# Performance work log

Measured on AMD Instinct MI355X. Metric: run time of the kernel, lower is better.

The kernel has to match this reference:

```python
import jax, jax.numpy as jnp
import numpy as np

# ---- static hyperparameters (mirror init_kwargs) ----
L_MAX = 3
N_MAX_L = [8, 6, 4, 2]            # radial basis size per l (precomputer.n_max_l)
N_CHANNELS = 32                   # num_element_channels
K_MAX_L = [n * N_CHANNELS for n in N_MAX_L]   # [256, 192, 128, 64]
SH_SIZES = [2 * l + 1 for l in range(L_MAX + 1)]  # [1,3,5,7]
MP_SCALING = 0.1
NU_SCALING = 0.1
NU_MAX = 2                        # max_correlation_order_per_layer
N_LAYERS = 2                      # num_message_passing_layers

# Fixed CG coupling tensors for all valid (l1, l2, L) with |l1-l2|<=L<=min(l1+l2, L_MAX).
# (Deterministic stand-ins for real Clebsch-Gordan coefficients; same sparsity/coupling
# structure and identical in fwd and fwdbwd modules.)
_rng = np.random.RandomState(0)
CG = {}
for _l1 in range(L_MAX + 1):
    for _l2 in range(L_MAX + 1):
        for _L in range(abs(_l1 - _l2), min(_l1 + _l2, L_MAX) + 1):
            CG[(_l1, _l2, _L)] = jnp.asarray(
                (_rng.randn(2 * _l1 + 1, 2 * _l2 + 1, 2 * _L + 1) * 0.2).astype(np.float32))


def split_l(x, sizes):
    out, i = [], 0
    for s in sizes:
        out.append(x[:, i:i + s])
        i += s
    return out


def embed_centers(feats, emb):
    # feats[l]: [N, 2l+1, n_l*C]; multiply channel block c by per-atom embedding emb[:, c]
    C = emb.shape[1]
    out = []
    for f in feats:
        n, m, k = f.shape
        out.append((f.reshape(n, m, k // C, C) * emb[:, None, None, :]).reshape(n, m, k))
    return out


def tensor_product(A, B):
    # per-atom CG tensor product, channel-aligned with truncation to min k
    n = A[0].shape[0]
    out = [jnp.zeros((n, 2 * L + 1, K_MAX_L[L]), A[0].dtype) for L in range(L_MAX + 1)]
    for (l1, l2, L), cg in CG.items():
        kk = min(K_MAX_L[l1], K_MAX_L[l2], K_MAX_L[L])
        t = jnp.einsum('nak,nbk,abM->nMk', A[l1][:, :, :kk], B[l2][:, :, :kk], cg)
        out[L] = out[L].at[:, :, :kk].add(t)
    return out


def cg_iterate(feats):
    # CGIterator: nu_max-1 iterated tensor products with residual accumulation
    g = feats
    for _ in range(NU_MAX - 1):
        tp = tensor_product(g, feats)
        g = [g[l] + NU_SCALING * tp[l] for l in range(L_MAX + 1)]
    return g


def invariant_mp(rb_l, sh_l, centers, emb_nbr, n_atoms):
    # spherical expansion: scatter rb x sh x neighbor-embedding over pairs -> centers
    out = []
    for l in range(L_MAX + 1):
        # [P, 2l+1, n_l, C] -> [P, 2l+1, k_l]
        msg = sh_l[l][:, :, None, None] * rb_l[l][:, None, :, None] * emb_nbr[:, None, None, :]
        msg = msg.reshape(msg.shape[0], 2 * l + 1, -1)
        out.append(MP_SCALING * jax.ops.segment_sum(msg, centers, num_segments=n_atoms))
    return out


def equivariant_mp(rb_l, sh_l, centers, neighbors, feats, n_atoms):
    # pair messages: CG-couple radially weighted SH edge features with neighbor features
    edge = [sh_l[l] * rb_l[l].sum(-1, keepdims=True) for l in range(L_MAX + 1)]  # [P, 2l+1]
    out = [jnp.zeros((n_atoms, 2 * L + 1, K_MAX_L[L]), feats[0].dtype) for L in range(L_MAX + 1)]
    for (l1, l2, L), cg in CG.items():
        kk = min(K_MAX_L[l2], K_MAX_L[L])
        w = jnp.einsum('pa,abM->pbM', edge[l1], cg)        # [P, 2l2+1, 2L+1]
        fg = feats[l2][neighbors, :, :kk]                   # gather: [P, 2l2+1, kk]
        msg = jnp.einsum('pbM,pbk->pMk', w, fg)             # [P, 2L+1, kk]
        out[L] = out[L].at[:, :, :kk].add(
            MP_SCALING * jax.ops.segment_sum(msg, centers, num_segments=n_atoms))
    return out


def setup_inputs() -> dict:
    key = jax.random.key(0)
    ks = jax.random.split(key, 8)
    N, P = 5000, 100000
    return {
        'sh': jax.random.normal(ks[0], (P, sum(SH_SIZES)), dtype=jnp.float32),
        'rb': jax.random.uniform(ks[1], (P, sum(N_MAX_L)), dtype=jnp.float32),
        'emb_table': jax.random.normal(ks[2], (4, N_CHANNELS), dtype=jnp.float32),
        'w_energy': jax.random.normal(ks[3], (K_MAX_L[0], 1), dtype=jnp.float32) * 0.05,
        'b_energy': jax.random.normal(ks[4], (1,), dtype=jnp.float32),
        'species_idx': jax.random.randint(ks[5], (N,), 0, 4, dtype=jnp.int32),
        'centers': jax.random.randint(ks[6], (P,), 0, N, dtype=jnp.int32),
        'neighbors': jax.random.randint(ks[7], (P,), 0, N, dtype=jnp.int32),
    }


def reference(sh, rb, emb_table, w_energy, b_energy, species_idx, centers, neighbors):
    n_atoms = species_idx.shape[0]
    sh_l = split_l(sh * NU_SCALING, SH_SIZES)   # nu_scaling applied to spherical harmonics
    rb_l = split_l(rb, N_MAX_L)
    center_emb = emb_table[species_idx]          # [N, C]
    emb_nbr = center_emb[neighbors]              # [P, C]
    # invariant message passing -> spherical expansion, then first CG iteration
    feats = invariant_mp(rb_l, sh_l, centers, emb_nbr, n_atoms)
    feats = cg_iterate(feats)
    # remaining equivariant message-passing layers
    for _ in range(N_LAYERS - 1):
        ef = embed_centers(feats, center_emb)
        mp = equivariant_mp(rb_l, sh_l, centers, neighbors, ef, n_atoms)
        feats = cg_iterate(mp)
    feats = embed_centers(feats, center_emb)
    energies = feats[0] @ w_energy + b_energy    # [N, 1, 1]
    return energies
```

## Files before the change

kernel.cpp:

```cpp
#include <hip/hip_runtime.h>
#include <vector>
#include <cmath>
#include <cstdint>

constexpr int KLc[4]  = {256,192,128,64};
constexpr int NMLc[4] = {8,6,4,2};
constexpr int SHBc[5] = {0,1,4,9,16};
constexpr int RBBc[5] = {0,8,14,18,20};
constexpr int FBc[5]  = {0,256,832,1472,1920};
constexpr int NCMB = 34, CGTOT = 3436, FTOT = 1920;

struct Combos { int l1[NCMB], l2[NCMB], L[NCMB], cgoff[NCMB], kk[NCMB]; };
constexpr Combos make_combos(){
  Combos c{}; int n=0, cg=0;
  for(int a=0;a<=3;a++)for(int b=0;b<=3;b++){
    int lo=a>b?a-b:b-a, hi=(a+b<3)?(a+b):3;
    for(int L=lo;L<=hi;L++){
      c.l1[n]=a; c.l2[n]=b; c.L[n]=L; c.cgoff[n]=cg;
      int mx=a>b?a:b; if(L>mx) mx=L; c.kk[n]=KLc[mx];
      cg+=(2*a+1)*(2*b+1)*(2*L+1); n++;
    }
  }
  return c;
}
constexpr Combos CB = make_combos();
static_assert(CB.cgoff[NCMB-1] + 7*7*7 == CGTOT, "cg size");

struct Grp { int cnt[4]; int list[4][12]; };
constexpr Grp make_Lg(){ Grp g{}; for(int i=0;i<NCMB;i++){ int L=CB.L[i]; g.list[L][g.cnt[L]++]=i; } return g; }
constexpr Grp LG = make_Lg();

struct Rows { int sh[64], rb[64], off[64]; };
constexpr Rows make_rows(){ Rows r{}; int i=0;
  for(int l=0;l<4;l++)for(int m=0;m<2*l+1;m++)for(int n=0;n<NMLc[l];n++){
    r.sh[i]=SHBc[l]+m; r.rb[i]=RBBc[l]+n; r.off[i]=FBc[l]+m*KLc[l]+n*32; i++; }
  for(;i<64;i++){ r.sh[i]=0; r.rb[i]=0; r.off[i]=0; }
  return r; }
constexpr Rows RWS = make_rows();

constexpr int NSL=425, NG=8, MAXS=56, MAXR=12, RPAD=149;

constexpr int iabs_(int x){ return x<0?-x:x; }
__host__ __device__ constexpr bool sl_valid(int l1,int l2,int kt){ return l2<=3-kt && iabs_(l1-l2)<=3-kt; }

__host__ __device__ constexpr int rb_base(int kt,int l1,int l2){
  int base=0;
  for(int p=0;p<4;p++)for(int q=0;q<4;q++){
    if(p==l1 && q==l2) return base;
    if(sl_valid(p,q,kt)) base += (2*p+1)*(2*q+1);
  }
  return base;
}

struct EqTab {
  int ns[NG];
  unsigned char eidx[NG][MAXS];
  unsigned char fidx[NG][MAXS];
  short         srow[NG][MAXS];
  unsigned char sph [NG][MAXS];
  int nr[NG];
  short roff[NG][MAXR];
  int total;
};
constexpr EqTab make_eqtab(){
  EqTab T{}; int gidx=0;
  for(int l2=0;l2<4;l2++)for(int kt=0;kt<4-l2;kt++)for(int b=0;b<2*l2+1;b++){
    const int rowoff = FBc[l2] + b*KLc[l2] + kt*64;
    for(int l1=0;l1<4;l1++){
      if(!sl_valid(l1,l2,kt)) continue;
      for(int a=0;a<2*l1+1;a++){
        int g = (gidx*NG)/NSL;
        int s = T.ns[g]++;
        T.eidx[g][s] = (unsigned char)(SHBc[l1]+a);
        int rbi = rb_base(kt,l1,l2) + a*(2*l2+1) + b;
        int ph, sr;
        if(kt==0){ if(l1<=2){ ph=0; sr=rbi; } else { ph=1; sr=rbi-144; } }
        else { ph=kt+1; sr=rbi; }
        T.sph[g][s]=(unsigned char)ph; T.srow[g][s]=(short)sr;
        int ri=-1;
        for(int r=0;r<T.nr[g];r++) if(T.roff[g][r]==(short)rowoff) ri=r;
        if(ri<0){ ri=T.nr[g]; T.roff[g][T.nr[g]++]=(short)rowoff; }
        T.fidx[g][s]=(unsigned char)ri;
        gidx++;
      }
    }
  }
  T.total=gidx;
  return T;
}
constexpr EqTab ET = make_eqtab();
static_assert(ET.total==NSL, "slice count");
constexpr bool chk_ns(){ for(int g=0;g<NG;g++) if(ET.ns[g]>MAXS) return false; return true; }
constexpr bool chk_nr(){ for(int g=0;g<NG;g++) if(ET.nr[g]>MAXR) return false; return true; }
static_assert(chk_ns(), "MAXS");
static_assert(chk_nr(), "MAXR");

struct CAsg { int cnt[NG]; unsigned char ci[NG][8]; };
constexpr CAsg make_casg(){
  CAsg C{}; bool used[NCMB]{}; int load[NG]{};
  for(int it=0; it<NCMB; it++){
    int best=-1, bc=-1;
    for(int i=0;i<NCMB;i++) if(!used[i]){
      int c=(2*CB.l1[i]+1)*(2*CB.l2[i]+1)*(2*CB.L[i]+1);
      if(c>bc){bc=c;best=i;}
    }
    used[best]=true;
    int g=0; for(int j=1;j<NG;j++) if(load[j]<load[g]) g=j;
    C.ci[g][C.cnt[g]++]=(unsigned char)best; load[g]+=bc;
  }
  return C;
}
constexpr CAsg CA = make_casg();
constexpr bool chk_ca(){ for(int g=0;g<NG;g++) if(CA.cnt[g]>8) return false; return true; }
static_assert(chk_ca(), "CA cap");

__host__ __device__ constexpr bool combo_in_phase(int ci,int ph){
  int l1=CB.l1[ci], l2=CB.l2[ci], L=CB.L[ci];
  if(ph==0) return l1<=2;
  if(ph==1) return l1==3;
  int kt=ph-1;
  return (l2<=3-kt) && (L<=3-kt);
}
__host__ __device__ constexpr int phase_kt(int ph){ return ph<=1?0:ph-1; }
__host__ __device__ constexpr int phase_rbadj(int ph){ return ph==1?144:0; }

namespace nprng {
struct MT {
  uint32_t mt[624]; int mti; bool has_g; double g;
  void seed(uint32_t s){ for(int i=0;i<624;i++){ mt[i]=s; s=1812433253u*(s^(s>>30))+(uint32_t)i+1u; } mti=624; has_g=false; g=0.0; }
  uint32_t u32(){
    if(mti>=624){
      for(int i=0;i<624;i++){
        uint32_t y=(mt[i]&0x80000000u)|(mt[(i+1)%624]&0x7fffffffu);
        mt[i]=mt[(i+397)%624]^(y>>1)^((y&1u)?0x9908b0dfu:0u);
      }
      mti=0;
    }
    uint32_t y=mt[mti++];
    y^=y>>11; y^=(y<<7)&0x9d2c5680u; y^=(y<<15)&0xefc60000u; y^=y>>18;
    return y;
  }
  double dbl(){ uint32_t a=u32()>>5, b=u32()>>6; return (a*67108864.0+b)/9007199254740992.0; }
  double gauss(){
    if(has_g){ has_g=false; return g; }
    double f,x1,x2,r2;
    do{ x1=2.0*dbl()-1.0; x2=2.0*dbl()-1.0; r2=x1*x1+x2*x2; }while(r2>=1.0||r2==0.0);
    f=sqrt(-2.0*log(r2)/r2);
    g=f*x1; has_g=true; return f*x2;
  }
};
}
static std::vector<float> build_cg(){
  nprng::MT r; r.seed(0);
  std::vector<float> v; v.reserve(CGTOT);
  for(int l1=0;l1<=3;l1++)for(int l2=0;l2<=3;l2++){
    int lo = l1>l2? l1-l2 : l2-l1;
    int hi = (l1+l2<3)? (l1+l2) : 3;
    for(int L=lo;L<=hi;L++){
      int n=(2*l1+1)*(2*l2+1)*(2*L+1);
      for(int i=0;i<n;i++) v.push_back((float)(r.gauss()*0.2));
    }
  }
  return v;
}

__global__ __launch_bounds__(256) void k_cemb(const float* __restrict__ emb_table,
    const int* __restrict__ species, float* __restrict__ cemb, int* __restrict__ counts, int N){
  int i = blockIdx.x*256 + threadIdx.x;
  if(i < N) counts[i] = 0;
  if(i < N*32){ int n = i>>5, c = i&31; cemb[i] = emb_table[species[n]*32 + c]; }
}

__global__ __launch_bounds__(256) void k_hist(const int* __restrict__ centers, int* counts, int P){
  int i = blockIdx.x*256 + threadIdx.x;
  if(i < P) atomicAdd(&counts[centers[i]], 1);
}

__global__ __launch_bounds__(256) void k_scan(const int* __restrict__ counts,
    int* __restrict__ offsets, int* __restrict__ cursor, int N){
  __shared__ int part[256];
  const int t = threadIdx.x;
  const int CH = (N + 255)/256;
  const int lo = t*CH;
  int hi = (t+1)*CH; if(hi > N) hi = N;
  int s = 0;
  for(int i=lo;i<hi;i++) s += counts[i];
  part[t] = s; __syncthreads();
  const int own = s;
  for(int d=1; d<256; d<<=1){
    int v = (t>=d)? part[t-d] : 0;
    __syncthreads();
    part[t] += v;
    __syncthreads();
  }
  int run = part[t] - own;
  for(int i=lo;i<hi;i++){ offsets[i]=run; cursor[i]=run; run += counts[i]; }
  if(t==255) offsets[N] = part[255];
}

__global__ __launch_bounds__(256) void k_scatter(const int* __restrict__ centers,
    int* cursor, int* __restrict__ perm, int P){
  int i = blockIdx.x*256 + threadIdx.x;
  if(i < P){ int c = centers[i]; int pos = atomicAdd(&cursor[c], 1); perm[pos] = i; }
}

__global__ __launch_bounds__(256) void k_inv(const float* __restrict__ sh, const float* __restrict__ rb,
    const float* __restrict__ cemb, const int* __restrict__ nbrs, const int* __restrict__ offsets,
    const int* __restrict__ perm, float* __restrict__ feats){
  const int a = blockIdx.x, t = threadIdx.x;
  __shared__ float sh_s[8][16], rb_s[8][20], emb_s[8][32], shrb_s[8][60];
  const int c = t & 31, rg = t >> 5;
  float acc[8];
  #pragma unroll
  for(int j=0;j<8;j++) acc[j] = 0.f;
  const int beg = offsets[a], cnt = offsets[a+1]-beg;
  for(int jb=0; jb<cnt; jb+=8){
    __syncthreads();
    for(int u=t; u<8*36; u+=256){
      int j=u/36, i=u-36*j;
      if(jb+j<cnt){
        int p=perm[beg+jb+j];
        if(i<16) sh_s[j][i]=sh[p*16+i]*0.1f;
        else     rb_s[j][i-16]=rb[p*20+i-16];
      }
    }
    for(int u=t; u<8*32; u+=256){
      int j=u>>5, i=u&31;
      if(jb+j<cnt){ int nb=nbrs[perm[beg+jb+j]]; emb_s[j][i]=cemb[(size_t)nb*32+i]; }
    }
    __syncthreads();
    for(int u=t; u<8*60; u+=256){
      int j=u/60, r=u-60*j;
      if(jb+j<cnt) shrb_s[j][r] = sh_s[j][RWS.sh[r]] * rb_s[j][RWS.rb[r]];
    }
    __syncthreads();
    const int jm = (cnt-jb<8)?(cnt-jb):8;
    for(int j=0;j<jm;j++){
      const float e = emb_s[j][c];
      #pragma unroll
      for(int q=0;q<8;q++){ int r=rg+8*q; if(r<60) acc[q]=fmaf(shrb_s[j][r], e, acc[q]); }
    }
  }
  #pragma unroll
  for(int q=0;q<8;q++){
    int r = rg + 8*q;
    if(r < 60) feats[(size_t)a*FTOT + RWS.off[r] + c] = 0.1f * acc[q];
  }
}

__device__ __forceinline__ float cg_u(const float* __restrict__ cg, int idx){
  return cg[__builtin_amdgcn_readfirstlane(idx)];
}
__global__ __launch_bounds__(256) void k_tp(float* __restrict__ feats, const float* __restrict__ cg){
  const int a = blockIdx.x, t = threadIdx.x;
  __shared__ float f_s[FTOT];
  float* fa = feats + (size_t)a*FTOT;
  for(int i=t;i<FTOT;i+=256)  f_s[i]  = fa[i];
  __syncthreads();
  #pragma unroll
  for(int L=0; L<4; L++){
    const int KLL = KLc[L], nL = 2*L+1;
    const int nel = nL*KLL;
    for(int e=t; e<nel; e+=256){
      const int M = e / KLL, k = e - M*KLL;
      float acc = 0.f;
      #pragma unroll
      for(int gi=0; gi<LG.cnt[L]; gi++){
        const int ci = LG.list[L][gi];
        const int l1 = CB.l1[ci], l2 = CB.l2[ci];
        if(k < CB.kk[ci]){
          const int n2 = 2*l2+1;
          #pragma unroll
          for(int aa=0; aa<2*l1+1; aa++){
            const float Av = f_s[FBc[l1] + aa*KLc[l1] + k];
            #pragma unroll
            for(int b=0; b<n2; b++)
              acc += cg_u(cg, CB.cgoff[ci] + (aa*n2+b)*nL + M) * (Av * f_s[FBc[l2] + b*KLc[l2] + k]);
          }
        }
      }
      fa[FBc[L] + M*KLL + k] = f_s[FBc[L] + M*KLL + k] + 0.1f*acc;
    }
  }
}

template<int G,int PH,int U>
__device__ __forceinline__ void contract_combos(const float* __restrict__ stageT,
    float* __restrict__ out_s, const float* __restrict__ cg, int lane){
  if constexpr (U < CA.cnt[G]) {
    constexpr int ci = CA.ci[G][U];
    if constexpr (combo_in_phase(ci,PH)) {
      constexpr int l1=CB.l1[ci], l2=CB.l2[ci], L=CB.L[ci];
      constexpr int n1=2*l1+1, n2=2*l2+1, nL=2*L+1;
      constexpr int kt=phase_kt(PH);
      constexpr int rbase = rb_base(kt,l1,l2) - phase_rbadj(PH);
      float oa[nL];
      #pragma unroll
      for(int M=0;M<nL;M++) oa[M]=0.f;
      #pragma unroll
      for(int aa=0;aa<n1;aa++){
        #pragma unroll
        for(int b=0;b<n2;b++){
          const float sv = stageT[lane*RPAD + rbase + aa*n2 + b];
          #pragma unroll
          for(int M=0;M<nL;M++)
            oa[M] = fmaf(cg[CB.cgoff[ci] + (aa*n2+b)*nL + M], sv, oa[M]);
        }
      }
      #pragma unroll
      for(int M=0;M<nL;M++)
        atomicAdd(&out_s[FBc[L] + M*KLc[L] + kt*64 + lane], oa[M]);
    }
    contract_combos<G,PH,U+1>(stageT,out_s,cg,lane);
  }
}

template<int G,int PH>
__device__ __forceinline__ void eq_phase(const float* acc, float* stageT, float* out_s,
    const float* __restrict__ cg, int lane){
  __syncthreads();
  #pragma unroll
  for(int s=0;s<ET.ns[G];s++){
    if(ET.sph[G][s]==PH) stageT[lane*RPAD + ET.srow[G][s]] = acc[s];
  }
  __syncthreads();
  contract_combos<G,PH,0>(stageT,out_s,cg,lane);
}

template<int G>
__device__ __forceinline__ void eq_group_main(
    const int a, const int t, const int lane,
    const float* __restrict__ sh, const float* __restrict__ rb,
    const float* __restrict__ cemb, const int* __restrict__ nbrs,
    const int* __restrict__ offsets, const int* __restrict__ perm,
    const float* __restrict__ featsA, float* __restrict__ featsB,
    const float* __restrict__ cg,
    float* stageT, float* out_s, float* edge_s, int* nb_s){
  constexpr int NS = ET.ns[G], NR = ET.nr[G];
  float acc[NS];
  #pragma unroll
  for(int s=0;s<NS;s++) acc[s]=0.f;
  for(int i=t;i<FTOT;i+=512) out_s[i]=0.f;
  const int beg = offsets[a], cnt = offsets[a+1]-beg;
  float fg_c[NR], ce_c = 0.f;
  if(cnt > 0){
    const int nb0 = nbrs[perm[beg]];
    ce_c = cemb[(size_t)nb0*32 + (lane&31)];
    const float* fp = featsA + (size_t)nb0*FTOT + lane;
    #pragma unroll
    for(int r=0;r<NR;r++) fg_c[r] = fp[ET.roff[G][r]];
  }
  for(int jb=0; jb<cnt; jb+=16){
    __syncthreads();
    if(t < 256){
      int j=t>>4, i=t&15;
      if(jb+j<cnt){
        int p = perm[beg+jb+j];
        if(i==0) nb_s[j] = nbrs[p];
        int l = (i==0)?0:(i<4)?1:(i<9)?2:3;
        float s=0.f;
        for(int n=RBBc[l]; n<RBBc[l+1]; n++) s += rb[p*20+n];
        edge_s[j*16+i] = sh[p*16+i]*0.1f*s;
      }
    }
    __syncthreads();
    const int jm = (cnt-jb<16)?(cnt-jb):16;
    for(int j=0;j<jm;j++){
      int nb_n = 0; bool have_n = true;
      if(j+1 < jm)            nb_n = nb_s[j+1];
      else if(jb+16 < cnt)    nb_n = nbrs[perm[beg+jb+16]];
      else                    have_n = false;
      float fg_n[NR], ce_n = 0.f;
      {
        const int nbl = have_n ? nb_n : 0;
        ce_n = cemb[(size_t)nbl*32 + (lane&31)];
        const float* fp = featsA + (size_t)nbl*FTOT + lane;
        #pragma unroll
        for(int r=0;r<NR;r++) fg_n[r] = fp[ET.roff[G][r]];
      }
      float ed[16];
      #pragma unroll
      for(int q=0;q<4;q++){
        float4 v = *(const float4*)(edge_s + j*16 + q*4);
        ed[q*4]=v.x; ed[q*4+1]=v.y; ed[q*4+2]=v.z; ed[q*4+3]=v.w;
      }
      float fgc[NR];
      #pragma unroll
      for(int r=0;r<NR;r++) fgc[r] = fg_c[r]*ce_c;
      #pragma unroll
      for(int s=0;s<NS;s++)
        acc[s] = fmaf(ed[ET.eidx[G][s]], fgc[ET.fidx[G][s]], acc[s]);
      #pragma unroll
      for(int r=0;r<NR;r++) fg_c[r] = fg_n[r];
      ce_c = ce_n;
    }
  }
  eq_phase<G,0>(acc,stageT,out_s,cg,lane);
  eq_phase<G,1>(acc,stageT,out_s,cg,lane);
  eq_phase<G,2>(acc,stageT,out_s,cg,lane);
  eq_phase<G,3>(acc,stageT,out_s,cg,lane);
  eq_phase<G,4>(acc,stageT,out_s,cg,lane);
  __syncthreads();
  float* ob = featsB + (size_t)a*FTOT;
  for(int i=t;i<FTOT;i+=512) ob[i] = 0.1f*out_s[i];
}

__global__ __launch_bounds__(512,4) void k_eq2(const float* __restrict__ sh, const float* __restrict__ rb,
    const float* __restrict__ cemb, const int* __restrict__ nbrs, const int* __restrict__ offsets,
    const int* __restrict__ perm, const float* __restrict__ featsA, float* __restrict__ featsB,
    const float* __restrict__ cg){
  __shared__ float stageT[64*RPAD];
  __shared__ float out_s[FTOT];
  __shared__ float edge_s[16*16];
  __shared__ int   nb_s[16];
  const int a = blockIdx.x, t = threadIdx.x, lane = t&63, g = t>>6;
  switch(g){
    case 0: eq_group_main<0>(a,t,lane,sh,rb,cemb,nbrs,offsets,perm,featsA,featsB,cg,stageT,out_s,edge_s,nb_s); break;
    case 1: eq_group_main<1>(a,t,lane,sh,rb,cemb,nbrs,offsets,perm,featsA,featsB,cg,stageT,out_s,edge_s,nb_s); break;
    case 2: eq_group_main<2>(a,t,lane,sh,rb,cemb,nbrs,offsets,perm,featsA,featsB,cg,stageT,out_s,edge_s,nb_s); break;
    case 3: eq_group_main<3>(a,t,lane,sh,rb,cemb,nbrs,offsets,perm,featsA,featsB,cg,stageT,out_s,edge_s,nb_s); break;
    case 4: eq_group_main<4>(a,t,lane,sh,rb,cemb,nbrs,offsets,perm,featsA,featsB,cg,stageT,out_s,edge_s,nb_s); break;
    case 5: eq_group_main<5>(a,t,lane,sh,rb,cemb,nbrs,offsets,perm,featsA,featsB,cg,stageT,out_s,edge_s,nb_s); break;
    case 6: eq_group_main<6>(a,t,lane,sh,rb,cemb,nbrs,offsets,perm,featsA,featsB,cg,stageT,out_s,edge_s,nb_s); break;
    default: eq_group_main<7>(a,t,lane,sh,rb,cemb,nbrs,offsets,perm,featsA,featsB,cg,stageT,out_s,edge_s,nb_s); break;
  }
}

__global__ __launch_bounds__(256) void k_energy(const float* __restrict__ feats,
    const float* __restrict__ cemb, const float* __restrict__ wE, const float* __restrict__ bE,
    float* __restrict__ out, int N){
  const int wid = threadIdx.x >> 6, lane = threadIdx.x & 63;
  const int a = blockIdx.x*4 + wid;
  if(a >= N) return;
  const float e = cemb[(size_t)a*32 + (lane & 31)];
  float s = 0.f;
  for(int k=lane; k<256; k+=64) s += feats[(size_t)a*FTOT + k] * e * wE[k];
  #pragma unroll
  for(int off=32; off; off>>=1) s += __shfl_down(s, off, 64);
  if(lane == 0) out[a] = s + bE[0];
}

extern "C" void kernel_launch(void* const* d_in, const int* in_sizes, int n_in,
                              void* d_out, int out_size, void* d_ws, size_t ws_size,
                              hipStream_t stream){
  const float* sh        = (const float*)d_in[0];
  const float* rb        = (const float*)d_in[1];
  const float* emb_table = (const float*)d_in[2];
  const float* wE        = (const float*)d_in[3];
  const float* bE        = (const float*)d_in[4];
  const int*   species   = (const int*)d_in[5];
  const int*   centers   = (const int*)d_in[6];
  const int*   nbrs      = (const int*)d_in[7];
  const int N = in_sizes[5];
  const int P = in_sizes[6];

  char* ws = (char*)d_ws; size_t off = 0;
  auto carve = [&](size_t bytes)->void*{
    void* p = ws + off; off = (off + bytes + 255) & ~(size_t)255; return p;
  };
  float* cg_d    = (float*)carve((size_t)CGTOT*4);
  float* cemb    = (float*)carve((size_t)N*32*4);
  int*   counts  = (int*)  carve((size_t)N*4);
  int*   offsets = (int*)  carve((size_t)(N+1)*4);
  int*   cursor  = (int*)  carve((size_t)N*4);
  int*   perm    = (int*)  carve((size_t)P*4);
  float* featsA  = (float*)carve((size_t)N*FTOT*4);
  float* featsB  = (float*)carve((size_t)N*FTOT*4);
  (void)ws_size; (void)n_in; (void)out_size;

  static const std::vector<float> cg_host = build_cg();
  hipMemcpyAsync(cg_d, cg_host.data(), (size_t)CGTOT*4, hipMemcpyHostToDevice, stream);

  k_cemb   <<<(N*32 + 255)/256, 256, 0, stream>>>(emb_table, species, cemb, counts, N);
  k_hist   <<<(P + 255)/256,    256, 0, stream>>>(centers, counts, P);
  k_scan   <<<1,                256, 0, stream>>>(counts, offsets, cursor, N);
  k_scatter<<<(P + 255)/256,    256, 0, stream>>>(centers, cursor, perm, P);
  k_inv    <<<N,                256, 0, stream>>>(sh, rb, cemb, nbrs, offsets, perm, featsA);
  k_tp     <<<N,                256, 0, stream>>>(featsA, cg_d);
  k_eq2    <<<N,                512, 0, stream>>>(sh, rb, cemb, nbrs, offsets, perm, featsA, featsB, cg_d);
  k_tp     <<<N,                256, 0, stream>>>(featsB, cg_d);
  k_energy <<<(N + 3)/4,        256, 0, stream>>>(featsB, cemb, wE, bE, (float*)d_out, N);
}
```

Before: 936.8 us.

## Split equivariant MP across 16 wavefronts with triple-buffered neighbor prefetch and pre-permuted edges

Doubles the number of slice groups in k_eq2 to 16 wavefronts (1024 threads per block), which halves the accumulator slices held per wave. A new k_permute kernel precomputes edge coefficients and neighbor indices in sorted order, so the main kernel no longer does the perm/rb gathers. The neighbor feature loads are triple-buffered to hide global-memory latency. Slices are sorted by edge index so each edge value is read from shared memory once. The costs are an extra kernel launch and buffer, and a 1024-thread block that may be harder to keep resident. stageT at 64*RPAD is unchanged, which matters if the staging code assumed 8 groups.

```diff
diff --git a/kernel.cpp b/kernel.cpp
--- a/kernel.cpp
+++ b/kernel.cpp
@@ -38,7 +38,8 @@
   return r; }
 constexpr Rows RWS = make_rows();
 
-constexpr int NSL=425, NG=8, MAXS=56, MAXR=12, RPAD=149;
+constexpr int NSL=425, NG=16, MAXS=28, MAXR=6, RPAD=149;
+constexpr int JB=48;
 
 constexpr int iabs_(int x){ return x<0?-x:x; }
 __host__ __device__ constexpr bool sl_valid(int l1,int l2,int kt){ return l2<=3-kt && iabs_(l1-l2)<=3-kt; }
@@ -86,6 +87,17 @@
     }
   }
   T.total=gidx;
+  for(int g=0;g<NG;g++){
+    for(int i=1;i<T.ns[g];i++){
+      unsigned char e=T.eidx[g][i], f=T.fidx[g][i], p=T.sph[g][i]; short r=T.srow[g][i];
+      int k=i-1;
+      while(k>=0 && T.eidx[g][k]>e){
+        T.eidx[g][k+1]=T.eidx[g][k]; T.fidx[g][k+1]=T.fidx[g][k];
+        T.sph[g][k+1]=T.sph[g][k];   T.srow[g][k+1]=T.srow[g][k]; k--;
+      }
+      T.eidx[g][k+1]=e; T.fidx[g][k+1]=f; T.sph[g][k+1]=p; T.srow[g][k+1]=r;
+    }
+  }
   return T;
 }
 constexpr EqTab ET = make_eqtab();
@@ -202,6 +214,20 @@
     int* cursor, int* __restrict__ perm, int P){
   int i = blockIdx.x*256 + threadIdx.x;
   if(i < P){ int c = centers[i]; int pos = atomicAdd(&cursor[c], 1); perm[pos] = i; }
+}
+
+__global__ __launch_bounds__(256) void k_permute(const float* __restrict__ sh,
+    const float* __restrict__ rb, const int* __restrict__ nbrs, const int* __restrict__ perm,
+    float* __restrict__ edge_p, int* __restrict__ nbrp, int P){
+  int u = blockIdx.x*256 + threadIdx.x;
+  int pos = u>>4, i = u&15;
+  if(pos >= P) return;
+  int p = perm[pos];
+  if(i==0) nbrp[pos] = nbrs[p];
+  int l = (i==0)?0:(i<4)?1:(i<9)?2:3;
+  float s=0.f;
+  for(int n=RBBc[l]; n<RBBc[l+1]; n++) s += rb[p*20+n];
+  edge_p[(size_t)pos*16+i] = sh[p*16+i]*0.1f*s;
 }
 
 __global__ __launch_bounds__(256) void k_inv(const float* __restrict__ sh, const float* __restrict__ rb,
@@ -328,11 +354,35 @@
 }
 
 template<int G>
+__device__ __forceinline__ void eq_load_pair(float* fg, float& ce, int nb, int lane,
+    const float* __restrict__ featsA, const float* __restrict__ cemb){
+  ce = cemb[(size_t)nb*32 + (lane&31)];
+  const float* fp = featsA + (size_t)nb*FTOT + lane;
+  #pragma unroll
+  for(int r=0;r<ET.nr[G];r++) fg[r] = fp[ET.roff[G][r]];
+}
+
+template<int G>
+__device__ __forceinline__ void eq_compute_pair(float* acc, const float* fg, float ce,
+    const float* edge_row){
+  constexpr int NR = ET.nr[G];
+  float fgc[NR];
+  #pragma unroll
+  for(int r=0;r<NR;r++) fgc[r] = fg[r]*ce;
+  float edv = 0.f;
+  #pragma unroll
+  for(int s=0;s<ET.ns[G];s++){
+    if(s==0 || ET.eidx[G][s]!=ET.eidx[G][s-1])
+      edv = edge_row[ET.eidx[G][s]];
+    acc[s] = fmaf(edv, fgc[ET.fidx[G][s]], acc[s]);
+  }
+}
+
+template<int G>
 __device__ __forceinline__ void eq_group_main(
     const int a, const int t, const int lane,
-    const float* __restrict__ sh, const float* __restrict__ rb,
-    const float* __restrict__ cemb, const int* __restrict__ nbrs,
-    const int* __restrict__ offsets, const int* __restrict__ perm,
+    const float* __restrict__ edge_p, const int* __restrict__ nbrp,
+    const float* __restrict__ cemb, const int* __restrict__ offsets,
     const float* __restrict__ featsA, float* __restrict__ featsB,
     const float* __restrict__ cg,
     float* stageT, float* out_s, float* edge_s, int* nb_s){
@@ -340,59 +390,35 @@
   float acc[NS];
   #pragma unroll
   for(int s=0;s<NS;s++) acc[s]=0.f;
-  for(int i=t;i<FTOT;i+=512) out_s[i]=0.f;
+  for(int i=t;i<FTOT;i+=1024) out_s[i]=0.f;
   const int beg = offsets[a], cnt = offsets[a+1]-beg;
-  float fg_c[NR], ce_c = 0.f;
-  if(cnt > 0){
-    const int nb0 = nbrs[perm[beg]];
-    ce_c = cemb[(size_t)nb0*32 + (lane&31)];
-    const float* fp = featsA + (size_t)nb0*FTOT + lane;
-    #pragma unroll
-    for(int r=0;r<NR;r++) fg_c[r] = fp[ET.roff[G][r]];
-  }
-  for(int jb=0; jb<cnt; jb+=16){
-    __syncthreads();
-    if(t < 256){
-      int j=t>>4, i=t&15;
-      if(jb+j<cnt){
-        int p = perm[beg+jb+j];
-        if(i==0) nb_s[j] = nbrs[p];
-        int l = (i==0)?0:(i<4)?1:(i<9)?2:3;
-        float s=0.f;
-        for(int n=RBBc[l]; n<RBBc[l+1]; n++) s += rb[p*20+n];
-        edge_s[j*16+i] = sh[p*16+i]*0.1f*s;
-      }
-    }
-    __syncthreads();
-    const int jm = (cnt-jb<16)?(cnt-jb):16;
-    for(int j=0;j<jm;j++){
-      int nb_n = 0; bool have_n = true;
-      if(j+1 < jm)            nb_n = nb_s[j+1];
-      else if(jb+16 < cnt)    nb_n = nbrs[perm[beg+jb+16]];
-      else                    have_n = false;
-      float fg_n[NR], ce_n = 0.f;
-      {
-        const int nbl = have_n ? nb_n : 0;
-        ce_n = cemb[(size_t)nbl*32 + (lane&31)];
-        const float* fp = featsA + (size_t)nbl*FTOT + lane;
-        #pragma unroll
-        for(int r=0;r<NR;r++) fg_n[r] = fp[ET.roff[G][r]];
-      }
-      float ed[16];
-      #pragma unroll
-      for(int q=0;q<4;q++){
-        float4 v = *(const float4*)(edge_s + j*16 + q*4);
-        ed[q*4]=v.x; ed[q*4+1]=v.y; ed[q*4+2]=v.z; ed[q*4+3]=v.w;
-      }
-      float fgc[NR];
-      #pragma unroll
-      for(int r=0;r<NR;r++) fgc[r] = fg_c[r]*ce_c;
-      #pragma unroll
-      for(int s=0;s<NS;s++)
-        acc[s] = fmaf(ed[ET.eidx[G][s]], fgc[ET.fidx[G][s]], acc[s]);
-      #pragma unroll
-      for(int r=0;r<NR;r++) fg_c[r] = fg_n[r];
-      ce_c = ce_n;
+  float fgA[NR], fgB[NR], fgC[NR]; float ceA=0.f, ceB=0.f, ceC=0.f;
+  { int nb = (0<cnt)? nbrp[beg+0] : 0; eq_load_pair<G>(fgA, ceA, nb, lane, featsA, cemb); }
+  { int nb = (1<cnt)? nbrp[beg+1] : 0; eq_load_pair<G>(fgB, ceB, nb, lane, featsA, cemb); }
+  { int nb = (2<cnt)? nbrp[beg+2] : 0; eq_load_pair<G>(fgC, ceC, nb, lane, featsA, cemb); }
+  for(int jb=0; jb<cnt; jb+=JB){
+    __syncthreads();
+    if(t < JB*16){
+      int j = t>>4;
+      if(jb+j < cnt) edge_s[t] = edge_p[(size_t)(beg+jb)*16 + t];
+    }
+    if(t < JB) nb_s[t] = (jb+t < cnt) ? nbrp[beg+jb+t] : 0;
+    __syncthreads();
+    const int jm = (cnt-jb<JB)?(cnt-jb):JB;
+    for(int j=0;j<jm;j+=3){
+      eq_compute_pair<G>(acc, fgA, ceA, edge_s + j*16);
+      { int q=jb+j+3; int nb=(q<cnt)?((q-jb<JB)? nb_s[q-jb] : nbrp[beg+q]):0;
+        eq_load_pair<G>(fgA, ceA, nb, lane, featsA, cemb); }
+      if(j+1<jm){
+        eq_compute_pair<G>(acc, fgB, ceB, edge_s + (j+1)*16);
+        int q=jb+j+4; int nb=(q<cnt)?((q-jb<JB)? nb_s[q-jb] : nbrp[beg+q]):0;
+        eq_load_pair<G>(fgB, ceB, nb, lane, featsA, cemb);
+      }
+      if(j+2<jm){
+        eq_compute_pair<G>(acc, fgC, ceC, edge_s + (j+2)*16);
+        int q=jb+j+5; int nb=(q<cnt)?((q-jb<JB)? nb_s[q-jb] : nbrp[beg+q]):0;
+        eq_load_pair<G>(fgC, ceC, nb, lane, featsA, cemb);
+      }
     }
   }
   eq_phase<G,0>(acc,stageT,out_s,cg,lane);
@@ -402,27 +428,35 @@
   eq_phase<G,4>(acc,stageT,out_s,cg,lane);
   __syncthreads();
   float* ob = featsB + (size_t)a*FTOT;
-  for(int i=t;i<FTOT;i+=512) ob[i] = 0.1f*out_s[i];
-}
-
-__global__ __launch_bounds__(512,4) void k_eq2(const float* __restrict__ sh, const float* __restrict__ rb,
-    const float* __restrict__ cemb, const int* __restrict__ nbrs, const int* __restrict__ offsets,
-    const int* __restrict__ perm, const float* __restrict__ featsA, float* __restrict__ featsB,
-    const float* __restrict__ cg){
+  for(int i=t;i<FTOT;i+=1024) ob[i] = 0.1f*out_s[i];
+}
+
+__global__ __launch_bounds__(1024,8) void k_eq2(const float* __restrict__ edge_p,
+    const int* __restrict__ nbrp, const float* __restrict__ cemb,
+    const int* __restrict__ offsets, const float* __restrict__ featsA,
+    float* __restrict__ featsB, const float* __restrict__ cg){
   __shared__ float stageT[64*RPAD];
   __shared__ float out_s[FTOT];
-  __shared__ float edge_s[16*16];
-  __shared__ int   nb_s[16];
+  __shared__ float edge_s[JB*16];
+  __shared__ int   nb_s[JB];
   const int a = blockIdx.x, t = threadIdx.x, lane = t&63, g = t>>6;
   switch(g){
-    case 0: eq_group_main<0>(a,t,lane,sh,rb,cemb,nbrs,offsets,perm,featsA,featsB,cg,stageT,out_s,edge_s,nb_s); break;
-    case 1: eq_group_main<1>(a,t,lane,sh,rb,cemb,nbrs,offsets,perm,featsA,featsB,cg,stageT,out_s,edge_s,nb_s); break;
-    case 2: eq_group_main<2>(a,t,lane,sh,rb,cemb,nbrs,offsets,perm,featsA,featsB,cg,stageT,out_s,edge_s,nb_s); break;
-    case 3: eq_group_main<3>(a,t,lane,sh,rb,cemb,nbrs,offsets,perm,featsA,featsB,cg,stageT,out_s,edge_s,nb_s); break;
-    case 4: eq_group_main<4>(a,t,lane,sh,rb,cemb,nbrs,offsets,perm,featsA,featsB,cg,stageT,out_s,edge_s,nb_s); break;
-    case 5: eq_group_main<5>(a,t,lane,sh,rb,cemb,nbrs,offsets,perm,featsA,featsB,cg,stageT,out_s,edge_s,nb_s); break;
-    case 6: eq_group_main<6>(a,t,lane,sh,rb,cemb,nbrs,offsets,perm,featsA,featsB,cg,stageT,out_s,edge_s,nb_s); break;
-    default: eq_group_main<7>(a,t,lane,sh,rb,cemb,nbrs,offsets,perm,featsA,featsB,cg,stageT,out_s,edge_s,nb_s); break;
+    case 0:  eq_group_main<0 >(a,t,lane,edge_p,nbrp,cemb,offsets,featsA,featsB,cg,stageT,out_s,edge_s,nb_s); break;
+    case 1:  eq_group_main<1 >(a,t,lane,edge_p,nbrp,cemb,offsets,featsA,featsB,cg,stageT,out_s,edge_s,nb_s); break;
+    case 2:  eq_group_main<2 >(a,t,lane,edge_p,nbrp,cemb,offsets,featsA,featsB,cg,stageT,out_s,edge_s,nb_s); break;
+    case 3:  eq_group_main<3 >(a,t,lane,edge_p,nbrp,cemb,offsets,featsA,featsB,cg,stageT,out_s,edge_s,nb_s); break;
+    case 4:  eq_group_main<4 >(a,t,lane,edge_p,nbrp,cemb,offsets,featsA,featsB,cg,stageT,out_s,edge_s,nb_s); break;
+    case 5:  eq_group_main<5 >(a,t,lane,edge_p,nbrp,cemb,offsets,featsA,featsB,cg,stageT,out_s,edge_s,nb_s); break;
+    case 6:  eq_group_main<6 >(a,t,lane,edge_p,nbrp,cemb,offsets,featsA,featsB,cg,stageT,out_s,edge_s,nb_s); break;
+    case 7:  eq_group_main<7 >(a,t,lane,edge_p,nbrp,cemb,offsets,featsA,featsB,cg,stageT,out_s,edge_s,nb_s); break;
+    case 8:  eq_group_main<8 >(a,t,lane,edge_p,nbrp,cemb,offsets,featsA,featsB,cg,stageT,out_s,edge_s,nb_s); break;
+    case 9:  eq_group_main<9 >(a,t,lane,edge_p,nbrp,cemb,offsets,featsA,featsB,cg,stageT,out_s,edge_s,nb_s); break;
+    case 10: eq_group_main<10>(a,t,lane,edge_p,nbrp,cemb,offsets,featsA,featsB,cg,stageT,out_s,edge_s,nb_s); break;
+    case 11: eq_group_main<11>(a,t,lane,edge_p,nbrp,cemb,offsets,featsA,featsB,cg,stageT,out_s,edge_s,nb_s); break;
+    case 12: eq_group_main<12>(a,t,lane,edge_p,nbrp,cemb,offsets,featsA,featsB,cg,stageT,out_s,edge_s,nb_s); break;
+    case 13: eq_group_main<13>(a,t,lane,edge_p,nbrp,cemb,offsets,featsA,featsB,cg,stageT,out_s,edge_s,nb_s); break;
+    case 14: eq_group_main<14>(a,t,lane,edge_p,nbrp,cemb,offsets,featsA,featsB,cg,stageT,out_s,edge_s,nb_s); break;
+    default: eq_group_main<15>(a,t,lane,edge_p,nbrp,cemb,offsets,featsA,featsB,cg,stageT,out_s,edge_s,nb_s); break;
   }
 }
 
@@ -464,6 +498,8 @@
   int*   offsets = (int*)  carve((size_t)(N+1)*4);
   int*   cursor  = (int*)  carve((size_t)N*4);
   int*   perm    = (int*)  carve((size_t)P*4);
+  float* edge_pd = (float*)carve((size_t)P*16*4);
+  int*   nbrp    = (int*)  carve((size_t)P*4);
   float* featsA  = (float*)carve((size_t)N*FTOT*4);
   float* featsB  = (float*)carve((size_t)N*FTOT*4);
   (void)ws_size; (void)n_in; (void)out_size;
@@ -475,9 +511,10 @@
   k_hist   <<<(P + 255)/256,    256, 0, stream>>>(centers, counts, P);
   k_scan   <<<1,                256, 0, stream>>>(counts, offsets, cursor, N);
   k_scatter<<<(P + 255)/256,    256, 0, stream>>>(centers, cursor, perm, P);
+  k_permute<<<(P*16 + 255)/256, 256, 0, stream>>>(sh, rb, nbrs, perm, edge_pd, nbrp, P);
   k_inv    <<<N,                256, 0, stream>>>(sh, rb, cemb, nbrs, offsets, perm, featsA);
   k_tp     <<<N,                256, 0, stream>>>(featsA, cg_d);
-  k_eq2    <<<N,                512, 0, stream>>>(sh, rb, cemb, nbrs, offsets, perm, featsA, featsB, cg_d);
+  k_eq2    <<<N,               1024, 0, stream>>>(edge_pd, nbrp, cemb, offsets, featsA, featsB, cg_d);
   k_tp     <<<N,                256, 0, stream>>>(featsB, cg_d);
   k_energy <<<(N + 3)/4,        256, 0, stream>>>(featsB, cemb, wE, bE, (float*)d_out, N);
 }
```

Result: slower. 1.207 ms (+28.9%).
